# Optimization experiments

Hardware: AMD Instinct MI355X
Metric: run time of the kernel (lower is better)

The kernel has to match this reference:

```python
import jax, jax.numpy as jnp
import numpy as np

B, LQ, LKV, D = 32, 1024, 1024, 512

def setup_inputs() -> dict:
    key = jax.random.key(0)
    kq, kkv = jax.random.split(key)
    query = jax.random.normal(kq, (B, LQ, D), dtype=jnp.float32)
    key_value = jax.random.normal(kkv, (B, LKV, D), dtype=jnp.float32)
    return {"query": query, "key_value": key_value}

def reference(query, key_value):
    # scores: [B, Lq, Lkv] (unscaled dot-product attention)
    scores = jnp.einsum('bqd,bkd->bqk', query, key_value)
    attn_score = jax.nn.softmax(scores, axis=-1)
    # output: [B, Lq, D]
    output = jnp.einsum('bqk,bkd->bqd', attn_score, key_value)
    return (output, attn_score)
```

## Files before the change

### kernel.cpp

```cpp
#include <hip/hip_runtime.h>


constexpr int NB  = 32;
constexpr int LQ  = 1024;
constexpr int LKV = 1024;
constexpr int DD  = 512;
constexpr int NROWS = NB * LQ;

typedef __attribute__((ext_vector_type(4))) float f4;
typedef __attribute__((ext_vector_type(4))) float f32x4;
typedef __attribute__((ext_vector_type(4))) unsigned short u16x4;
typedef __attribute__((ext_vector_type(8))) __bf16 bf16x8;

__device__ __forceinline__ unsigned short f2bf(float x) {
  unsigned u = __builtin_bit_cast(unsigned, x);
  unsigned r = u + 0x7FFFu + ((u >> 16) & 1u);
  return (unsigned short)(r >> 16);
}
__device__ __forceinline__ float bf2f(unsigned short h) {
  unsigned u = ((unsigned)h) << 16;
  return __builtin_bit_cast(float, u);
}

__device__ __forceinline__ void gload16(const void* g, void* l) {
  __builtin_amdgcn_global_load_lds((const __attribute__((address_space(1))) unsigned int*)g,
                                   (__attribute__((address_space(3))) unsigned int*)l,
                                   16, 0, 0);
}

constexpr int PAD = 40;

__global__ __launch_bounds__(256) void prep_all_kernel(const float* __restrict__ Q,
                                                       const float* __restrict__ KV,
                                                       unsigned short* __restrict__ Qh,
                                                       unsigned short* __restrict__ Ql,
                                                       unsigned short* __restrict__ Kh,
                                                       unsigned short* __restrict__ Kl,
                                                       unsigned short* __restrict__ KVT)
{
  __shared__ unsigned short T[64][72];
  const int b  = blockIdx.z;
  const int tk = blockIdx.y;
  const int td = blockIdx.x;
  const int tid = threadIdx.x;

#pragma unroll
  for (int i = 0; i < 4; ++i) {
    int idx = tid + i * 256;
    int r   = idx >> 4;
    int c4  = (idx & 15) << 2;
    size_t goff = ((size_t)b * LKV + tk * 64 + r) * DD + td * 64 + c4;
    f4 v = *(const f4*)(KV + goff);
    u16x4 h, l;
#pragma unroll
    for (int u = 0; u < 4; ++u) {
      h[u] = f2bf(v[u]);
      l[u] = f2bf(v[u] - bf2f(h[u]));
    }
    *(u16x4*)&T[r][c4] = h;
    *(u16x4*)(Kh + goff) = h;
    *(u16x4*)(Kl + goff) = l;

    f4 q = *(const f4*)(Q + goff);
    u16x4 qh, ql;
#pragma unroll
    for (int u = 0; u < 4; ++u) {
      qh[u] = f2bf(q[u]);
      ql[u] = f2bf(q[u] - bf2f(qh[u]));
    }
    *(u16x4*)(Qh + goff) = qh;
    *(u16x4*)(Ql + goff) = ql;
  }
  __syncthreads();

#pragma unroll
  for (int i = 0; i < 4; ++i) {
    int idx = tid + i * 256;
    int c   = idx >> 4;
    int r4  = (idx & 15) << 2;
    u16x4 w = { T[r4][c], T[r4 + 1][c], T[r4 + 2][c], T[r4 + 3][c] };
    *(u16x4*)(KVT + ((size_t)b * DD + td * 64 + c) * LKV + tk * 64 + r4) = w;
  }
}

__global__ __launch_bounds__(256) void gemm_qk7_kernel(const unsigned short* __restrict__ Qh,
                                                       const unsigned short* __restrict__ Ql,
                                                       const unsigned short* __restrict__ Kh,
                                                       const unsigned short* __restrict__ Kl,
                                                       float* __restrict__ S,
                                                       float* __restrict__ Pmax,
                                                       float* __restrict__ Psum)
{
  __shared__ unsigned short SM[4][128 * 32];
  const int n       = blockIdx.x;
  const int logical = (n & 7) * 256 + (n >> 3);
  const int b   = logical >> 6;
  const int t   = logical & 63;
  const int ti  = t >> 3;
  const int tj  = t & 7;
  const int tid  = threadIdx.x;
  const int lane = tid & 63;
  const int wid  = tid >> 6;
  const int wr = (wid >> 1) * 64;
  const int wc = (wid & 1) * 64;

  const size_t qo = ((size_t)b * LQ  + ti * 128) * DD;
  const size_t ko = ((size_t)b * LKV + tj * 128) * DD;
  const unsigned short* tb =
      (wid == 0) ? Qh + qo : (wid == 1) ? Ql + qo : (wid == 2) ? Kh + ko : Kl + ko;

  const int lr  = lane >> 2;
  const int ssw = (lane & 3) ^ ((lr >> 1) & 3);

  const int l15 = lane & 15;
  const int swz = ((lane >> 4) ^ ((l15 >> 1) & 3)) << 3;

  f32x4 acc[4][4] = {};

  for (int it = 0; it < 16; ++it) {
    const int ks = it * 32;
    __syncthreads();
#pragma unroll
    for (int c = 0; c < 8; ++c) {
      const unsigned short* g = tb + (size_t)(c * 16 + lr) * DD + ks + ssw * 8;
      gload16(g, &SM[wid][c * 512]);
    }
    __syncthreads();

    bf16x8 ah[4], al[4], bh[4], bl[4];
#pragma unroll
    for (int m = 0; m < 4; ++m) {
      int off = (wr + m * 16 + l15) * 32 + swz;
      ah[m] = *(const bf16x8*)&SM[0][off];
      al[m] = *(const bf16x8*)&SM[1][off];
    }
#pragma unroll
    for (int nn = 0; nn < 4; ++nn) {
      int off = (wc + nn * 16 + l15) * 32 + swz;
      bh[nn] = *(const bf16x8*)&SM[2][off];
      bl[nn] = *(const bf16x8*)&SM[3][off];
    }
#pragma unroll
    for (int m = 0; m < 4; ++m)
#pragma unroll
      for (int nn = 0; nn < 4; ++nn)
        acc[m][nn] = __builtin_amdgcn_mfma_f32_16x16x32_bf16(ah[m], bh[nn], acc[m][nn], 0, 0, 0);
#pragma unroll
    for (int m = 0; m < 4; ++m)
#pragma unroll
      for (int nn = 0; nn < 4; ++nn)
        acc[m][nn] = __builtin_amdgcn_mfma_f32_16x16x32_bf16(ah[m], bl[nn], acc[m][nn], 0, 0, 0);
#pragma unroll
    for (int m = 0; m < 4; ++m)
#pragma unroll
      for (int nn = 0; nn < 4; ++nn)
        acc[m][nn] = __builtin_amdgcn_mfma_f32_16x16x32_bf16(al[m], bh[nn], acc[m][nn], 0, 0, 0);
  }

  float* Sb = S + (size_t)b * LQ * LKV;
#pragma unroll
  for (int m = 0; m < 4; ++m) {
    int row0 = ti * 128 + wr + m * 16 + ((lane >> 4) << 2);
#pragma unroll
    for (int nn = 0; nn < 4; ++nn) {
      int col = tj * 128 + wc + nn * 16 + (lane & 15);
#pragma unroll
      for (int j = 0; j < 4; ++j)
        Sb[(size_t)(row0 + j) * LKV + col] = acc[m][nn][j];
    }
  }

  const int g16  = lane >> 4;
  const int l16  = lane & 15;
  const int wcid = wc >> 6;
#pragma unroll
  for (int m = 0; m < 4; ++m) {
#pragma unroll
    for (int j = 0; j < 4; ++j) {
      float rm = fmaxf(fmaxf(acc[m][0][j], acc[m][1][j]), fmaxf(acc[m][2][j], acc[m][3][j]));
#pragma unroll
      for (int off = 8; off >= 1; off >>= 1)
        rm = fmaxf(rm, __shfl_xor(rm, off));
      float se = 0.f;
#pragma unroll
      for (int nn = 0; nn < 4; ++nn)
        se += __expf(acc[m][nn][j] - rm);
#pragma unroll
      for (int off = 8; off >= 1; off >>= 1)
        se += __shfl_xor(se, off);
      if (l16 == 0) {
        int row  = ti * 128 + wr + m * 16 + g16 * 4 + j;
        size_t p = ((size_t)b * LQ + row) * 16 + tj * 2 + wcid;
        Pmax[p] = rm;
        Psum[p] = se;
      }
    }
  }
}

__global__ __launch_bounds__(256) void reduce_stats_kernel(const float* __restrict__ Pmax,
                                                           const float* __restrict__ Psum,
                                                           float* __restrict__ M,
                                                           float* __restrict__ Inv)
{
  int row = blockIdx.x * 256 + threadIdx.x;
  const float* pm = Pmax + (size_t)row * 16;
  const float* ps = Psum + (size_t)row * 16;
  float mx = pm[0];
#pragma unroll
  for (int i = 1; i < 16; ++i) mx = fmaxf(mx, pm[i]);
  float s = 0.f;
#pragma unroll
  for (int i = 0; i < 16; ++i) s += ps[i] * __expf(pm[i] - mx);
  M[row]   = mx;
  Inv[row] = 1.0f / s;
}

__global__ __launch_bounds__(1024, 4) void gemm_av7_kernel(float* __restrict__ Sio,
                                                           const unsigned short* __restrict__ KVT,
                                                           const float* __restrict__ Mrow,
                                                           const float* __restrict__ Invr,
                                                           float* __restrict__ O)
{
  __shared__ unsigned short Asm[128][72];
  __shared__ unsigned short Bsm[512 * 64];
  __shared__ float Ms[128], Is[128];
  const int n       = blockIdx.x;
  const int logical = (n & 7) * 32 + (n >> 3);
  const int b  = logical >> 3;
  const int mi = logical & 7;
  const int tid  = threadIdx.x;
  const int lane = tid & 63;
  const int wid  = tid >> 6;
  const int wr  = (wid >> 2) * 32;
  const int wcb = (wid & 3) * 128;

  float* Sb = Sio + ((size_t)b * LQ + mi * 128) * LKV;
  const unsigned short* Bb = KVT + (size_t)b * DD * LKV;

  if (tid < 128) {
    int gr = b * LQ + mi * 128 + tid;
    Ms[tid] = Mrow[gr];
    Is[tid] = Invr[gr];
  }

  const int lr8 = lane >> 3;
  const int ssw = (lane & 7) ^ lr8;

  f32x4 acc[2][8] = {};

  for (int ks = 0; ks < LKV; ks += 64) {
    __syncthreads();
#pragma unroll
    for (int i = 0; i < 2; ++i) {
      int idx = tid + i * 1024;
      int r   = idx >> 4;
      int k4  = (idx & 15) << 2;
      float* ap = Sb + (size_t)r * LKV + ks + k4;
      f4 v = *(const f4*)ap;
      float mr = Ms[r], ir = Is[r];
      f4 p; u16x4 h;
#pragma unroll
      for (int u = 0; u < 4; ++u) {
        p[u] = __expf(v[u] - mr) * ir;
        h[u] = f2bf(p[u]);
      }
      *(f4*)ap = p;
      *(u16x4*)&Asm[r][k4] = h;
    }
#pragma unroll
    for (int c = 0; c < 4; ++c) {
      int cc = wid * 4 + c;
      int dd = cc * 8 + lr8;
      const unsigned short* g = Bb + (size_t)dd * LKV + ks + ssw * 8;
      gload16(g, &Bsm[cc * 512]);
    }
    __syncthreads();

#pragma unroll
    for (int kk = 0; kk < 64; kk += 32) {
      const int kf = kk + ((lane >> 4) << 3);
      const int cl = kf >> 3;
      bf16x8 af[2];
#pragma unroll
      for (int m = 0; m < 2; ++m)
        af[m] = *(const bf16x8*)&Asm[wr + m * 16 + (lane & 15)][kf];
#pragma unroll
      for (int h = 0; h < 2; ++h) {
        bf16x8 bfv[4];
#pragma unroll
        for (int nn = 0; nn < 4; ++nn) {
          int dd = wcb + (h * 4 + nn) * 16 + (lane & 15);
          int sp = cl ^ (dd & 7);
          bfv[nn] = *(const bf16x8*)&Bsm[dd * 64 + sp * 8];
        }
#pragma unroll
        for (int m = 0; m < 2; ++m)
#pragma unroll
          for (int nn = 0; nn < 4; ++nn)
            acc[m][h * 4 + nn] =
                __builtin_amdgcn_mfma_f32_16x16x32_bf16(af[m], bfv[nn], acc[m][h * 4 + nn], 0, 0, 0);
      }
    }
  }

  float* Ob = O + ((size_t)b * LQ + mi * 128) * DD;
#pragma unroll
  for (int m = 0; m < 2; ++m) {
    int r0 = wr + m * 16 + ((lane >> 4) << 2);
#pragma unroll
    for (int nn = 0; nn < 8; ++nn) {
      int col = wcb + nn * 16 + (lane & 15);
#pragma unroll
      for (int j = 0; j < 4; ++j)
        Ob[(size_t)(r0 + j) * DD + col] = acc[m][nn][j];
    }
  }
}

__global__ __launch_bounds__(256) void gemm_qk_kernel(const float* __restrict__ Q,
                                                      const float* __restrict__ KV,
                                                      float* __restrict__ S)
{
  __shared__ unsigned short Ah[128][PAD], Al[128][PAD], Bh[128][PAD], Bl[128][PAD];
  const int b   = blockIdx.y;
  const int ti  = blockIdx.x >> 3;
  const int tj  = blockIdx.x & 7;
  const int tid  = threadIdx.x;
  const int lane = tid & 63;
  const int wid  = tid >> 6;
  const int wr = (wid >> 1) * 64;
  const int wc = (wid & 1) * 64;

  const float* Qb = Q  + (size_t)b * LQ  * DD + (size_t)ti * 128 * DD;
  const float* Kb = KV + (size_t)b * LKV * DD + (size_t)tj * 128 * DD;

  f32x4 acc[4][4] = {};

  for (int ks = 0; ks < DD; ks += 32) {
    __syncthreads();
#pragma unroll
    for (int i = 0; i < 4; ++i) {
      int idx = tid + i * 256;
      int r   = idx >> 3;
      int k4  = (idx & 7) << 2;
      f4 qa = *(const f4*)(Qb + (size_t)r * DD + ks + k4);
      f4 ka = *(const f4*)(Kb + (size_t)r * DD + ks + k4);
      u16x4 qh, ql, kh, kl;
#pragma unroll
      for (int u = 0; u < 4; ++u) {
        unsigned short h = f2bf(qa[u]);
        qh[u] = h;  ql[u] = f2bf(qa[u] - bf2f(h));
        unsigned short h2 = f2bf(ka[u]);
        kh[u] = h2; kl[u] = f2bf(ka[u] - bf2f(h2));
      }
      *(u16x4*)&Ah[r][k4] = qh;  *(u16x4*)&Al[r][k4] = ql;
      *(u16x4*)&Bh[r][k4] = kh;  *(u16x4*)&Bl[r][k4] = kl;
    }
    __syncthreads();

    const int kf = (lane >> 4) << 3;
    bf16x8 ah[4], al[4], bh[4], bl[4];
#pragma unroll
    for (int m = 0; m < 4; ++m) {
      int row = wr + m * 16 + (lane & 15);
      ah[m] = *(const bf16x8*)&Ah[row][kf];
      al[m] = *(const bf16x8*)&Al[row][kf];
    }
#pragma unroll
    for (int n = 0; n < 4; ++n) {
      int row = wc + n * 16 + (lane & 15);
      bh[n] = *(const bf16x8*)&Bh[row][kf];
      bl[n] = *(const bf16x8*)&Bl[row][kf];
    }
#pragma unroll
    for (int m = 0; m < 4; ++m)
#pragma unroll
      for (int n = 0; n < 4; ++n) {
        acc[m][n] = __builtin_amdgcn_mfma_f32_16x16x32_bf16(ah[m], bh[n], acc[m][n], 0, 0, 0);
        acc[m][n] = __builtin_amdgcn_mfma_f32_16x16x32_bf16(ah[m], bl[n], acc[m][n], 0, 0, 0);
        acc[m][n] = __builtin_amdgcn_mfma_f32_16x16x32_bf16(al[m], bh[n], acc[m][n], 0, 0, 0);
      }
  }

  float* Sb = S + (size_t)b * LQ * LKV;
#pragma unroll
  for (int m = 0; m < 4; ++m) {
    int row0 = ti * 128 + wr + m * 16 + ((lane >> 4) << 2);
#pragma unroll
    for (int n = 0; n < 4; ++n) {
      int col = tj * 128 + wc + n * 16 + (lane & 15);
#pragma unroll
      for (int j = 0; j < 4; ++j)
        Sb[(size_t)(row0 + j) * LKV + col] = acc[m][n][j];
    }
  }
}

__global__ __launch_bounds__(256) void softmax_kernel(float* __restrict__ S)
{
  __shared__ float redmax[4], redsum[4];
  const int tid = threadIdx.x;
  float* p = S + (size_t)blockIdx.x * LKV;

  f4 v = *(const f4*)(p + tid * 4);
  float mx = fmaxf(fmaxf(v[0], v[1]), fmaxf(v[2], v[3]));
#pragma unroll
  for (int off = 32; off >= 1; off >>= 1)
    mx = fmaxf(mx, __shfl_xor(mx, off));
  if ((tid & 63) == 0) redmax[tid >> 6] = mx;
  __syncthreads();
  mx = fmaxf(fmaxf(redmax[0], redmax[1]), fmaxf(redmax[2], redmax[3]));

  f4 e;
#pragma unroll
  for (int u = 0; u < 4; ++u) e[u] = __expf(v[u] - mx);
  float sm = e[0] + e[1] + e[2] + e[3];
#pragma unroll
  for (int off = 32; off >= 1; off >>= 1)
    sm += __shfl_xor(sm, off);
  if ((tid & 63) == 0) redsum[tid >> 6] = sm;
  __syncthreads();
  sm = redsum[0] + redsum[1] + redsum[2] + redsum[3];

  float inv = 1.0f / sm;
  f4 o = { e[0] * inv, e[1] * inv, e[2] * inv, e[3] * inv };
  *(f4*)(p + tid * 4) = o;
}

__global__ __launch_bounds__(256) void kvt_prep_kernel(const float* __restrict__ KV,
                                                       unsigned short* __restrict__ KVT)
{
  __shared__ unsigned short T[64][72];
  const int b  = blockIdx.z;
  const int tk = blockIdx.y;
  const int td = blockIdx.x;
  const int tid = threadIdx.x;

#pragma unroll
  for (int i = 0; i < 4; ++i) {
    int idx = tid + i * 256;
    int r   = idx >> 4;
    int c4  = (idx & 15) << 2;
    f4 v = *(const f4*)(KV + ((size_t)b * LKV + tk * 64 + r) * DD + td * 64 + c4);
    u16x4 h;
#pragma unroll
    for (int u = 0; u < 4; ++u) h[u] = f2bf(v[u]);
    *(u16x4*)&T[r][c4] = h;
  }
  __syncthreads();

#pragma unroll
  for (int i = 0; i < 4; ++i) {
    int idx = tid + i * 256;
    int c   = idx >> 4;
    int r4  = (idx & 15) << 2;
    u16x4 w = { T[r4][c], T[r4 + 1][c], T[r4 + 2][c], T[r4 + 3][c] };
    *(u16x4*)(KVT + ((size_t)b * DD + td * 64 + c) * LKV + tk * 64 + r4) = w;
  }
}

__global__ __launch_bounds__(512) void gemm_av2_kernel(const float* __restrict__ A,
                                                       const unsigned short* __restrict__ KVT,
                                                       float* __restrict__ O)
{
  __shared__ unsigned short Asm[128][72];
  __shared__ unsigned short Bsm[256 * 64];
  const int b  = blockIdx.z;
  const int mi = blockIdx.y;
  const int nj = blockIdx.x;
  const int tid  = threadIdx.x;
  const int lane = tid & 63;
  const int wid  = tid >> 6;
  const int wr = (wid >> 2) * 64;
  const int wc = (wid & 3) * 64;

  const float* Ab = A + (size_t)b * LQ * LKV + (size_t)mi * 128 * LKV;
  const unsigned short* Bb = KVT + ((size_t)b * DD + nj * 256) * LKV;

  f32x4 acc[4][4] = {};

  for (int ks = 0; ks < LKV; ks += 64) {
    __syncthreads();
#pragma unroll
    for (int i = 0; i < 4; ++i) {
      int idx = tid + i * 512;
      int r   = idx >> 4;
      int k4  = (idx & 15) << 2;
      f4 v = *(const f4*)(Ab + (size_t)r * LKV + ks + k4);
      u16x4 h;
#pragma unroll
      for (int u = 0; u < 4; ++u) h[u] = f2bf(v[u]);
      *(u16x4*)&Asm[r][k4] = h;
    }
#pragma unroll
    for (int c = 0; c < 4; ++c) {
      int cc = wid * 4 + c;
      int dd = cc * 8 + (lane >> 3);
      int ss = (lane & 7) ^ (dd & 7);
      const unsigned short* g = Bb + (size_t)dd * LKV + ks + ss * 8;
      gload16(g, &Bsm[cc * 512]);
    }
    __syncthreads();

#pragma unroll
    for (int kk = 0; kk < 64; kk += 32) {
      const int kf = kk + ((lane >> 4) << 3);
      const int cl = kf >> 3;
      bf16x8 af[4], bfv[4];
#pragma unroll
      for (int m = 0; m < 4; ++m)
        af[m] = *(const bf16x8*)&Asm[wr + m * 16 + (lane & 15)][kf];
#pragma unroll
      for (int n = 0; n < 4; ++n) {
        int dd = wc + n * 16 + (lane & 15);
        int sp = cl ^ (dd & 7);
        bfv[n] = *(const bf16x8*)&Bsm[dd * 64 + sp * 8];
      }
#pragma unroll
      for (int m = 0; m < 4; ++m)
#pragma unroll
        for (int n = 0; n < 4; ++n)
          acc[m][n] = __builtin_amdgcn_mfma_f32_16x16x32_bf16(af[m], bfv[n], acc[m][n], 0, 0, 0);
    }
  }

  float* Ob = O + (size_t)b * LQ * DD;
#pragma unroll
  for (int m = 0; m < 4; ++m) {
    int row0 = mi * 128 + wr + m * 16 + ((lane >> 4) << 2);
#pragma unroll
    for (int n = 0; n < 4; ++n) {
      int col = nj * 256 + wc + n * 16 + (lane & 15);
#pragma unroll
      for (int j = 0; j < 4; ++j)
        Ob[(size_t)(row0 + j) * DD + col] = acc[m][n][j];
    }
  }
}

__global__ __launch_bounds__(256) void gemm_av_kernel(const float* __restrict__ A,
                                                      const float* __restrict__ KV,
                                                      float* __restrict__ O)
{
  __shared__ unsigned short Ab[128][PAD], Bt[128][PAD];
  const int b  = blockIdx.z;
  const int mi = blockIdx.y;
  const int nj = blockIdx.x;
  const int tid  = threadIdx.x;
  const int lane = tid & 63;
  const int wid  = tid >> 6;
  const int wr = (wid >> 1) * 64;
  const int wc = (wid & 1) * 64;

  const float* Arow = A  + (size_t)b * LQ * LKV + (size_t)mi * 128 * LKV;
  const float* Kb   = KV + (size_t)b * LKV * DD;

  f32x4 acc[4][4] = {};

  for (int ks = 0; ks < LKV; ks += 32) {
    __syncthreads();
#pragma unroll
    for (int i = 0; i < 4; ++i) {
      int idx = tid + i * 256;
      {
        int r  = idx >> 3;
        int k4 = (idx & 7) << 2;
        f4 av = *(const f4*)(Arow + (size_t)r * LKV + ks + k4);
        u16x4 h;
#pragma unroll
        for (int u = 0; u < 4; ++u) h[u] = f2bf(av[u]);
        *(u16x4*)&Ab[r][k4] = h;
      }
      {
        int kr = idx >> 5;
        int c4 = (idx & 31) << 2;
        f4 kv = *(const f4*)(Kb + (size_t)(ks + kr) * DD + nj * 128 + c4);
        unsigned short hv[4];
#pragma unroll
        for (int u = 0; u < 4; ++u) hv[u] = f2bf(kv[u]);
#pragma unroll
        for (int u = 0; u < 4; ++u) {
          int uu = (u + kr) & 3;
          Bt[c4 + uu][kr] = hv[uu];
        }
      }
    }
    __syncthreads();

    const int kf = (lane >> 4) << 3;
    bf16x8 af[4], bfv[4];
#pragma unroll
    for (int m = 0; m < 4; ++m)
      af[m] = *(const bf16x8*)&Ab[wr + m * 16 + (lane & 15)][kf];
#pragma unroll
    for (int n = 0; n < 4; ++n)
      bfv[n] = *(const bf16x8*)&Bt[wc + n * 16 + (lane & 15)][kf];
#pragma unroll
    for (int m = 0; m < 4; ++m)
#pragma unroll
      for (int n = 0; n < 4; ++n)
        acc[m][n] = __builtin_amdgcn_mfma_f32_16x16x32_bf16(af[m], bfv[n], acc[m][n], 0, 0, 0);
  }

  float* Ob = O + (size_t)b * LQ * DD;
#pragma unroll
  for (int m = 0; m < 4; ++m) {
    int row0 = mi * 128 + wr + m * 16 + ((lane >> 4) << 2);
#pragma unroll
    for (int n = 0; n < 4; ++n) {
      int col = nj * 128 + wc + n * 16 + (lane & 15);
#pragma unroll
      for (int j = 0; j < 4; ++j)
        Ob[(size_t)(row0 + j) * DD + col] = acc[m][n][j];
    }
  }
}

extern "C" void kernel_launch(void* const* d_in, const int* in_sizes, int n_in,
                              void* d_out, int out_size, void* d_ws, size_t ws_size,
                              hipStream_t stream) {
  const float* Q  = (const float*)d_in[0];
  const float* KV = (const float*)d_in[1];
  float* out  = (float*)d_out;
  float* attn = out + (size_t)NB * LQ * DD;

  const size_t NQ  = (size_t)NB * LQ * DD;
  const size_t big_bytes = 5 * NQ * sizeof(unsigned short);
  const size_t kvt_bytes = NQ * sizeof(unsigned short);

  if (ws_size >= big_bytes) {
    unsigned short* Qh  = (unsigned short*)d_ws;
    unsigned short* Qlo = Qh  + NQ;
    unsigned short* Kh  = Qlo + NQ;
    unsigned short* Kl  = Kh  + NQ;
    unsigned short* KVT = Kl  + NQ;
    float* Pmax = out;
    float* Psum = out + (size_t)NROWS * 16;
    float* Mrow = (float*)Kh;
    float* Invr = Mrow + NROWS;

    prep_all_kernel<<<dim3(DD / 64, LKV / 64, NB), 256, 0, stream>>>(Q, KV, Qh, Qlo, Kh, Kl, KVT);
    gemm_qk7_kernel<<<dim3(2048), 256, 0, stream>>>(Qh, Qlo, Kh, Kl, attn, Pmax, Psum);
    reduce_stats_kernel<<<NROWS / 256, 256, 0, stream>>>(Pmax, Psum, Mrow, Invr);
    gemm_av7_kernel<<<dim3(256), 1024, 0, stream>>>(attn, KVT, Mrow, Invr, out);
  } else if (ws_size >= kvt_bytes) {
    unsigned short* KVT = (unsigned short*)d_ws;
    gemm_qk_kernel<<<dim3(64, NB), 256, 0, stream>>>(Q, KV, attn);
    kvt_prep_kernel<<<dim3(DD / 64, LKV / 64, NB), 256, 0, stream>>>(KV, KVT);
    softmax_kernel<<<dim3(NB * LQ), 256, 0, stream>>>(attn);
    gemm_av2_kernel<<<dim3(DD / 256, LQ / 128, NB), 512, 0, stream>>>(attn, KVT, out);
  } else {
    gemm_qk_kernel<<<dim3(64, NB), 256, 0, stream>>>(Q, KV, attn);
    softmax_kernel<<<dim3(NB * LQ), 256, 0, stream>>>(attn);
    gemm_av_kernel<<<dim3(DD / 128, LQ / 128, NB), 256, 0, stream>>>(attn, KV, out);
  }
}
```

Baseline: 314.9 us.

## Load QK GEMM operands directly from global memory instead of LDS staging

The QK score GEMM stops staging Q/K hi-lo bf16 tiles through shared memory with barriers. Each wave now loads its MFMA fragments straight from global memory, relying on L1/L2 for reuse across waves. Launch bounds request three blocks per SM. This drops the LDS traffic and the two syncthreads per k-step, but each wave re-reads tiles that other waves also need, and the per-lane loads are 16-byte strided rows that coalesce less well.

```diff
diff --git a/kernel.cpp b/kernel.cpp
--- a/kernel.cpp
+++ b/kernel.cpp
@@ -83,15 +83,14 @@
   }
 }
 
-__global__ __launch_bounds__(256) void gemm_qk7_kernel(const unsigned short* __restrict__ Qh,
-                                                       const unsigned short* __restrict__ Ql,
-                                                       const unsigned short* __restrict__ Kh,
-                                                       const unsigned short* __restrict__ Kl,
-                                                       float* __restrict__ S,
-                                                       float* __restrict__ Pmax,
-                                                       float* __restrict__ Psum)
-{
-  __shared__ unsigned short SM[4][128 * 32];
+__global__ __launch_bounds__(256, 3) void gemm_qk8_kernel(const unsigned short* __restrict__ Qh,
+                                                          const unsigned short* __restrict__ Ql,
+                                                          const unsigned short* __restrict__ Kh,
+                                                          const unsigned short* __restrict__ Kl,
+                                                          float* __restrict__ S,
+                                                          float* __restrict__ Pmax,
+                                                          float* __restrict__ Psum)
+{
   const int n       = blockIdx.x;
   const int logical = (n & 7) * 256 + (n >> 3);
   const int b   = logical >> 6;
@@ -106,39 +105,34 @@
 
   const size_t qo = ((size_t)b * LQ  + ti * 128) * DD;
   const size_t ko = ((size_t)b * LKV + tj * 128) * DD;
-  const unsigned short* tb =
-      (wid == 0) ? Qh + qo : (wid == 1) ? Ql + qo : (wid == 2) ? Kh + ko : Kl + ko;
-
-  const int lr  = lane >> 2;
-  const int ssw = (lane & 3) ^ ((lr >> 1) & 3);
+  const unsigned short* Aq = Qh + qo;
+  const unsigned short* Al_ = Ql + qo;
+  const unsigned short* Bh_ = Kh + ko;
+  const unsigned short* Bl_ = Kl + ko;
 
   const int l15 = lane & 15;
-  const int swz = ((lane >> 4) ^ ((l15 >> 1) & 3)) << 3;
+  const int kf0 = (lane >> 4) << 3;
+
+  int rowA[4], rowB[4];
+#pragma unroll
+  for (int m = 0; m < 4; ++m) rowA[m] = (wr + m * 16 + l15) * DD + kf0;
+#pragma unroll
+  for (int nn = 0; nn < 4; ++nn) rowB[nn] = (wc + nn * 16 + l15) * DD + kf0;
 
   f32x4 acc[4][4] = {};
 
-  for (int it = 0; it < 16; ++it) {
-    const int ks = it * 32;
-    __syncthreads();
-#pragma unroll
-    for (int c = 0; c < 8; ++c) {
-      const unsigned short* g = tb + (size_t)(c * 16 + lr) * DD + ks + ssw * 8;
-      gload16(g, &SM[wid][c * 512]);
-    }
-    __syncthreads();
-
+#pragma unroll 2
+  for (int ks = 0; ks < DD; ks += 32) {
     bf16x8 ah[4], al[4], bh[4], bl[4];
 #pragma unroll
     for (int m = 0; m < 4; ++m) {
-      int off = (wr + m * 16 + l15) * 32 + swz;
-      ah[m] = *(const bf16x8*)&SM[0][off];
-      al[m] = *(const bf16x8*)&SM[1][off];
+      ah[m] = *(const bf16x8*)(Aq  + rowA[m] + ks);
+      al[m] = *(const bf16x8*)(Al_ + rowA[m] + ks);
     }
 #pragma unroll
     for (int nn = 0; nn < 4; ++nn) {
-      int off = (wc + nn * 16 + l15) * 32 + swz;
-      bh[nn] = *(const bf16x8*)&SM[2][off];
-      bl[nn] = *(const bf16x8*)&SM[3][off];
+      bh[nn] = *(const bf16x8*)(Bh_ + rowB[nn] + ks);
+      bl[nn] = *(const bf16x8*)(Bl_ + rowB[nn] + ks);
     }
 #pragma unroll
     for (int m = 0; m < 4; ++m)
@@ -641,7 +635,7 @@
     float* Invr = Mrow + NROWS;
 
     prep_all_kernel<<<dim3(DD / 64, LKV / 64, NB), 256, 0, stream>>>(Q, KV, Qh, Qlo, Kh, Kl, KVT);
-    gemm_qk7_kernel<<<dim3(2048), 256, 0, stream>>>(Qh, Qlo, Kh, Kl, attn, Pmax, Psum);
+    gemm_qk8_kernel<<<dim3(2048), 256, 0, stream>>>(Qh, Qlo, Kh, Kl, attn, Pmax, Psum);
     reduce_stats_kernel<<<NROWS / 256, 256, 0, stream>>>(Pmax, Psum, Mrow, Invr);
     gemm_av7_kernel<<<dim3(256), 1024, 0, stream>>>(attn, KVT, Mrow, Invr, out);
   } else if (ws_size >= kvt_bytes) {
```

Result: slower. 437.5 us (+38.9%).
